# Kernel tuning notes

Hardware: AMD Instinct MI355X
Metric: run time of the kernel (lower is better)

Reference implementation:

```python
import jax, jax.numpy as jnp
import numpy as np


def _lstm(x, Wk, Wr, b):
    # x: [B, T, D] -> hidden sequence [B, T, U] (Keras LSTM gate order i,f,c,o)
    B, T, D = x.shape
    U = Wr.shape[0]
    xz = jnp.einsum('btd,dk->btk', x, Wk) + b  # precompute input projection

    def step(carry, z_t):
        h, c = carry
        z = z_t + h @ Wr
        i, f, g, o = jnp.split(z, 4, axis=-1)
        i = jax.nn.sigmoid(i)
        f = jax.nn.sigmoid(f)
        g = jnp.tanh(g)
        o = jax.nn.sigmoid(o)
        c = f * c + i * g
        h = o * jnp.tanh(c)
        return (h, c), h

    h0 = jnp.zeros((B, U), x.dtype)
    (_, _), hs = jax.lax.scan(step, (h0, h0), jnp.swapaxes(xz, 0, 1))
    return jnp.swapaxes(hs, 0, 1)


def _bilstm(x, fk, fr, fb, bk, br, bb, return_sequences):
    fwd = _lstm(x, fk, fr, fb)
    bwd = _lstm(x[:, ::-1], bk, br, bb)
    if return_sequences:
        return jnp.concatenate([fwd, bwd[:, ::-1]], axis=-1)
    return jnp.concatenate([fwd[:, -1], bwd[:, -1]], axis=-1)


def setup_inputs() -> dict:
    key = jax.random.key(0)
    ks = jax.random.split(key, 20)
    B, T, H, M, F = 64, 512, 768, 50, 8
    s = 0.05
    inp = {
        'hidden': jax.random.normal(ks[0], (B, T, H), jnp.float32),
        'mask': jax.random.randint(ks[1], (B, T), 0, M, jnp.int32),
        'lstm_input': jax.random.normal(ks[2], (B, M, F), jnp.float32),
        'max_len': M,
        'l1f_k': s * jax.random.normal(ks[3], (H + F, 4 * 256), jnp.float32),
        'l1f_r': s * jax.random.normal(ks[4], (256, 4 * 256), jnp.float32),
        'l1f_b': jnp.zeros((4 * 256,), jnp.float32),
        'l1b_k': s * jax.random.normal(ks[5], (H + F, 4 * 256), jnp.float32),
        'l1b_r': s * jax.random.normal(ks[6], (256, 4 * 256), jnp.float32),
        'l1b_b': jnp.zeros((4 * 256,), jnp.float32),
        'l2f_k': s * jax.random.normal(ks[7], (512, 4 * 128), jnp.float32),
        'l2f_r': s * jax.random.normal(ks[8], (128, 4 * 128), jnp.float32),
        'l2f_b': jnp.zeros((4 * 128,), jnp.float32),
        'l2b_k': s * jax.random.normal(ks[9], (512, 4 * 128), jnp.float32),
        'l2b_r': s * jax.random.normal(ks[10], (128, 4 * 128), jnp.float32),
        'l2b_b': jnp.zeros((4 * 128,), jnp.float32),
        'd1_w': s * jax.random.normal(ks[11], (256, 128), jnp.float32),
        'd1_b': jnp.zeros((128,), jnp.float32),
        'd3_w': s * jax.random.normal(ks[12], (128, 64), jnp.float32),
        'd3_b': jnp.zeros((64,), jnp.float32),
        'd5_w': s * jax.random.normal(ks[13], (64, 32), jnp.float32),
        'd5_b': jnp.zeros((32,), jnp.float32),
        'd7_w': s * jax.random.normal(ks[14], (32, 1), jnp.float32),
        'd7_b': jnp.zeros((1,), jnp.float32),
    }
    return inp


def reference(hidden, mask, lstm_input, max_len,
              l1f_k, l1f_r, l1f_b, l1b_k, l1b_r, l1b_b,
              l2f_k, l2f_r, l2f_b, l2b_k, l2b_r, l2b_b,
              d1_w, d1_b, d3_w, d3_b, d5_w, d5_b, d7_w, d7_b):
    # Segment reduce: for each bin d in [0, max_len), sum hidden states whose
    # mask==d, divided by max_len (the original divides by max_len, not counts).
    onehot = (mask[:, :, None] == jnp.arange(max_len)[None, None, :]).astype(hidden.dtype)
    merged = jnp.einsum('btd,btm->bmd', hidden, onehot) / jnp.asarray(max_len, hidden.dtype)
    concat = jnp.concatenate([merged, lstm_input], axis=2)  # [B, max_len, 768+F]
    out = _bilstm(concat, l1f_k, l1f_r, l1f_b, l1b_k, l1b_r, l1b_b, True)   # [B, M, 512]
    out = _bilstm(out, l2f_k, l2f_r, l2f_b, l2b_k, l2b_r, l2b_b, False)      # [B, 256]
    out = jax.nn.relu(out @ d1_w + d1_b)
    out = jax.nn.relu(out @ d3_w + d3_b)
    out = jax.nn.relu(out @ d5_w + d5_b)
    return jax.nn.sigmoid(out @ d7_w + d7_b)  # [B, 1]
```

## Files before the change

kernel.cpp:

```cpp
#include <hip/hip_runtime.h>
#include <hip/hip_bf16.h>

typedef __attribute__((ext_vector_type(8))) short bf16x8;
typedef __attribute__((ext_vector_type(4))) float f32x4;
typedef __attribute__((ext_vector_type(4))) unsigned int u32x4;
typedef _Float16 half2_ __attribute__((ext_vector_type(2)));

__device__ __forceinline__ unsigned short f2bf(float f) {
    unsigned int x = __float_as_uint(f);
    x += 0x7fffu + ((x >> 16) & 1u);
    return (unsigned short)(x >> 16);
}

__device__ __forceinline__ float sigmoidf_(float x) {
    return 1.f / (1.f + __expf(-x));
}
__device__ __forceinline__ float tanhf_(float x) {
    float e = __expf(-2.f * fabsf(x));
    float t = (1.f - e) / (1.f + e);
    return copysignf(t, x);
}

__device__ __forceinline__ float fdot2_(unsigned int w, unsigned int h, float acc) {
#if __has_builtin(__builtin_amdgcn_fdot2)
    return __builtin_amdgcn_fdot2(__builtin_bit_cast(half2_, w),
                                  __builtin_bit_cast(half2_, h), acc, false);
#else
    half2_ a = __builtin_bit_cast(half2_, w);
    half2_ b = __builtin_bit_cast(half2_, h);
    return acc + (float)a.x * (float)b.x + (float)a.y * (float)b.y;
#endif
}

__device__ void convT_body(const float* __restrict__ srcF,
                           const float* __restrict__ srcB,
                           short* __restrict__ dst, int Ksrc, int Kpad,
                           int Nhalf, int bx, int by, float* tile ) {
    int k0 = bx * 64, n0 = by * 64;
    const float* src = (n0 < Nhalf) ? srcF : srcB;
    int ncol0 = (n0 < Nhalf) ? n0 : n0 - Nhalf;
    int c = threadIdx.x & 63;
    int r4 = threadIdx.x >> 6;
    for (int rr = r4; rr < 64; rr += 4) {
        int k = k0 + rr;
        tile[rr * 65 + c] = (k < Ksrc) ? src[(size_t)k * Nhalf + ncol0 + c] : 0.f;
    }
    __syncthreads();
    int rn = threadIdx.x >> 2, q = threadIdx.x & 3;
    short* d = dst + (size_t)(n0 + rn) * Kpad + k0 + q * 16;
    #pragma unroll
    for (int i = 0; i < 16; i++) d[i] = (short)f2bf(tile[(q * 16 + i) * 65 + rn]);
}

__device__ void conv_rec_pack_body(const float* __restrict__ WrF,
                                   const float* __restrict__ WrB,
                                   unsigned int* __restrict__ dst, int K, int N,
                                   int kq, int dir) {
    const float* src = dir ? WrB : WrF;
    int kqq = kq >> 2, q = kq & 3;
    for (int c = threadIdx.x; c < N; c += 256) {
        half2_ h;
        h.x = (_Float16)src[(size_t)(2 * kq) * N + c];
        h.y = (_Float16)src[(size_t)(2 * kq + 1) * N + c];
        dst[(((size_t)dir * (K / 8) + kqq) * N + c) * 4 + q] =
            __builtin_bit_cast(unsigned int, h);
    }
}

__device__ void onehot_body(const int* __restrict__ mask,
                            const float* __restrict__ lstm_in,
                            short* __restrict__ onehot,
                            short* __restrict__ concatB, int b) {
    int tid = threadIdx.x;
    short* oh = onehot + (size_t)b * 64 * 512;
    for (int i = tid; i < 64 * 512 / 8; i += 256) {
        bf16x8 z = {};
        *(bf16x8*)(oh + i * 8) = z;
    }
    __syncthreads();
    for (int t = tid; t < 512; t += 256) {
        unsigned int m = (unsigned int)mask[b * 512 + t];
        if (m < 50u) oh[(size_t)m * 512 + t] = (short)0x3F80;
    }
    for (int idx = tid; idx < 50 * 64; idx += 256) {
        int m = idx >> 6, q = idx & 63;
        float v = (q < 8) ? lstm_in[(b * 50 + m) * 8 + q] : 0.f;
        concatB[(size_t)(b * 50 + m) * 832 + 768 + q] = (short)f2bf(v);
    }
}

__global__ __launch_bounds__(256) void prep_all(
    const float* __restrict__ l1f_k, const float* __restrict__ l1b_k,
    short* __restrict__ wk1T,
    const float* __restrict__ l2f_k, const float* __restrict__ l2b_k,
    short* __restrict__ wk2T,
    const float* __restrict__ l1f_r, const float* __restrict__ l1b_r,
    unsigned int* __restrict__ wp1,
    const float* __restrict__ l2f_r, const float* __restrict__ l2b_r,
    unsigned int* __restrict__ wp2,
    const int* __restrict__ mask, const float* __restrict__ lstm_in,
    short* __restrict__ onehot, short* __restrict__ concatB) {
    __shared__ float tile[64 * 65];
    int blk = blockIdx.x;
    if (blk < 416) {
        convT_body(l1f_k, l1b_k, wk1T, 776, 832, 1024, blk % 13, blk / 13, tile);
    } else if (blk < 544) {
        int q = blk - 416;
        convT_body(l2f_k, l2b_k, wk2T, 512, 512, 512, q % 8, q / 8, tile);
    } else if (blk < 800) {
        int q = blk - 544;
        conv_rec_pack_body(l1f_r, l1b_r, wp1, 256, 1024, q & 127, q >> 7);
    } else if (blk < 928) {
        int q = blk - 800;
        conv_rec_pack_body(l2f_r, l2b_r, wp2, 128, 512, q & 63, q >> 6);
    } else {
        onehot_body(mask, lstm_in, onehot, concatB, blk - 928);
    }
}

__global__ __launch_bounds__(256) void seg_gemm(
    const float* __restrict__ hidden, const short* __restrict__ onehot,
    short* __restrict__ concatB) {
    int b = blockIdx.x, n0 = blockIdx.y * 64;
    __shared__ short Al[64][36];
    __shared__ short Bl[64][36];
    int tid = threadIdx.x;
    int lane = tid & 63, w = tid >> 6;
    int fr = lane & 15, fq = lane >> 4;
    int wc = w * 16;
    int arow = tid >> 2, apart = tid & 3;
    int nloc = tid & 63, kq = tid >> 6;

    f32x4 acc[4] = {};

    const short* ohb = onehot + (size_t)b * 64 * 512;
    const float* hbase = hidden + (size_t)b * 512 * 768 + n0 + nloc;

    bf16x8 aReg = *(const bf16x8*)(ohb + (size_t)arow * 512 + apart * 8);
    float bReg[8];
    #pragma unroll
    for (int kk = 0; kk < 8; kk++)
        bReg[kk] = hbase[(size_t)(kq * 8 + kk) * 768];

    for (int k0 = 0; k0 < 512; k0 += 32) {
        *(bf16x8*)&Al[arow][apart * 8] = aReg;
        #pragma unroll
        for (int kk = 0; kk < 8; kk += 2) {
            unsigned int pk = (unsigned int)f2bf(bReg[kk]) |
                              ((unsigned int)f2bf(bReg[kk + 1]) << 16);
            *(unsigned int*)&Bl[nloc][kq * 8 + kk] = pk;
        }
        __syncthreads();
        if (k0 + 32 < 512) {
            int kn = k0 + 32;
            aReg = *(const bf16x8*)(ohb + (size_t)arow * 512 + kn + apart * 8);
            #pragma unroll
            for (int kk = 0; kk < 8; kk++)
                bReg[kk] = hbase[(size_t)(kn + kq * 8 + kk) * 768];
        }
        bf16x8 af[4], bfv;
        #pragma unroll
        for (int mi = 0; mi < 4; mi++)
            af[mi] = *(const bf16x8*)&Al[mi * 16 + fr][fq * 8];
        bfv = *(const bf16x8*)&Bl[wc + fr][fq * 8];
        #pragma unroll
        for (int mi = 0; mi < 4; mi++)
            acc[mi] = __builtin_amdgcn_mfma_f32_16x16x32_bf16(af[mi], bfv,
                                                              acc[mi], 0, 0, 0);
        __syncthreads();
    }
    const float inv = 1.f / 50.f;
    #pragma unroll
    for (int mi = 0; mi < 4; mi++) {
        #pragma unroll
        for (int r = 0; r < 4; r++) {
            int m = mi * 16 + fq * 4 + r;
            if (m < 50) {
                int col = n0 + wc + fr;
                concatB[(size_t)(b * 50 + m) * 832 + col] =
                    (short)f2bf(acc[mi][r] * inv);
            }
        }
    }
}

__global__ __launch_bounds__(256) void gemm_bf16(
    const short* __restrict__ A, const short* __restrict__ BT,
    const float* __restrict__ biasF, const float* __restrict__ biasB, int Nhalf,
    float* __restrict__ C, int M, int N, int Kpad) {
    __shared__ short Al[128][72];
    __shared__ short Bl[128][72];
    int m0 = blockIdx.x * 128, n0 = blockIdx.y * 128;
    int tid = threadIdx.x;
    int lane = tid & 63, w = tid >> 6;
    int srow = tid >> 1, shalf = tid & 1;
    int wr = (w >> 1) * 64, wc = (w & 1) * 64;
    int fr = lane & 15, fq = lane >> 4;

    f32x4 acc[4][4] = {};

    const short* aPtr = A + (size_t)(m0 + srow) * Kpad + shalf * 32;
    const short* bPtr = BT + (size_t)(n0 + srow) * Kpad + shalf * 32;
    bf16x8 av0 = *(const bf16x8*)(aPtr);
    bf16x8 av1 = *(const bf16x8*)(aPtr + 16);
    bf16x8 bv0 = *(const bf16x8*)(bPtr);
    bf16x8 bv1 = *(const bf16x8*)(bPtr + 16);

    for (int k0 = 0; k0 < Kpad; k0 += 64) {
        *(bf16x8*)&Al[srow][shalf * 32] = av0;
        *(bf16x8*)&Al[srow][shalf * 32 + 16] = av1;
        *(bf16x8*)&Bl[srow][shalf * 32] = bv0;
        *(bf16x8*)&Bl[srow][shalf * 32 + 16] = bv1;
        __syncthreads();
        if (k0 + 64 < Kpad) {
            av0 = *(const bf16x8*)(aPtr + k0 + 64);
            av1 = *(const bf16x8*)(aPtr + k0 + 80);
            bv0 = *(const bf16x8*)(bPtr + k0 + 64);
            bv1 = *(const bf16x8*)(bPtr + k0 + 80);
        }
        #pragma unroll
        for (int ks = 0; ks < 2; ks++) {
            bf16x8 af[4], bfv[4];
            #pragma unroll
            for (int mi = 0; mi < 4; mi++)
                af[mi] = *(const bf16x8*)&Al[wr + mi * 16 + fr][ks * 32 + fq * 8];
            #pragma unroll
            for (int ni = 0; ni < 4; ni++)
                bfv[ni] = *(const bf16x8*)&Bl[wc + ni * 16 + fr][ks * 32 + fq * 8];
            #pragma unroll
            for (int mi = 0; mi < 4; mi++)
                #pragma unroll
                for (int ni = 0; ni < 4; ni++)
                    acc[mi][ni] = __builtin_amdgcn_mfma_f32_16x16x32_bf16(
                        af[mi], bfv[ni], acc[mi][ni], 0, 0, 0);
        }
        __syncthreads();
    }
    #pragma unroll
    for (int mi = 0; mi < 4; mi++)
        #pragma unroll
        for (int ni = 0; ni < 4; ni++) {
            #pragma unroll
            for (int r = 0; r < 4; r++) {
                int row = m0 + wr + mi * 16 + fq * 4 + r;
                int col = n0 + wc + ni * 16 + fr;
                float bias = (col < Nhalf) ? biasF[col] : biasB[col - Nhalf];
                C[(size_t)row * N + col] = acc[mi][ni][r] + bias;
            }
        }
}

#define R1_REG 25
#define R1_LDS 7

__global__ __attribute__((amdgpu_flat_work_group_size(512, 512)))
__attribute__((amdgpu_waves_per_eu(2, 2))) void lstm_rec1(
    const float* __restrict__ xz, const unsigned int* __restrict__ wp,
    short* __restrict__ out1) {
    int b = blockIdx.x >> 1, dir = blockIdx.x & 1;
    const unsigned int* wd = wp + (size_t)dir * 32 * 1024 * 4;
    extern __shared__ char smem[];
    unsigned int* Wl = (unsigned int*)smem;
    unsigned int* h2u = (unsigned int*)(smem + R1_LDS * 1024 * 16);
    float* zbuf = (float*)(smem + R1_LDS * 1024 * 16 + 512);
    int tid = threadIdx.x;
    int lane = tid & 63;
    int cA = tid, cB = tid + 512;

    unsigned int wA[R1_REG * 4], wB[R1_REG * 4];
    #pragma unroll
    for (int g = 0; g < R1_REG; g++) {
        u32x4 ta = *(const u32x4*)&wd[((size_t)g * 1024 + cA) * 4];
        u32x4 tb = *(const u32x4*)&wd[((size_t)g * 1024 + cB) * 4];
        wA[g * 4 + 0] = ta.x; wA[g * 4 + 1] = ta.y;
        wA[g * 4 + 2] = ta.z; wA[g * 4 + 3] = ta.w;
        wB[g * 4 + 0] = tb.x; wB[g * 4 + 1] = tb.y;
        wB[g * 4 + 2] = tb.z; wB[g * 4 + 3] = tb.w;
    }
    #pragma unroll
    for (int g = 0; g < R1_REG; g++) {
        asm volatile("" : "+v"(wA[g * 4 + 0]), "+v"(wA[g * 4 + 1]),
                          "+v"(wA[g * 4 + 2]), "+v"(wA[g * 4 + 3]),
                          "+v"(wB[g * 4 + 0]), "+v"(wB[g * 4 + 1]),
                          "+v"(wB[g * 4 + 2]), "+v"(wB[g * 4 + 3]));
    }
    #pragma unroll
    for (int g = 0; g < R1_LDS; g++) {
        *(u32x4*)&Wl[(g * 1024 + cA) * 4] =
            *(const u32x4*)&wd[((size_t)(R1_REG + g) * 1024 + cA) * 4];
        *(u32x4*)&Wl[(g * 1024 + cB) * 4] =
            *(const u32x4*)&wd[((size_t)(R1_REG + g) * 1024 + cB) * 4];
    }
    if (tid < 128) h2u[tid] = 0u;
    float cstate = 0.f;
    __syncthreads();

    for (int s = 0; s < 50; s++) {
        int tt = dir ? 49 - s : s;
        const float* xrow = xz + (size_t)(b * 50 + tt) * 2048 + dir * 1024;
        float xA = xrow[cA];
        float xB = xrow[cB];
        float zA0 = 0.f, zA1 = 0.f, zA2 = 0.f, zA3 = 0.f;
        float zB0 = 0.f, zB1 = 0.f, zB2 = 0.f, zB3 = 0.f;
        unsigned int hv0 = h2u[lane];
        unsigned int hv1 = h2u[lane + 64];
        #pragma unroll
        for (int g = 0; g < R1_REG; g++) {
            unsigned int src = (g < 16) ? hv0 : hv1;
            int base = (g < 16) ? 4 * g : 4 * (g - 16);
            unsigned int h0 = __builtin_amdgcn_readlane(src, base + 0);
            unsigned int h1 = __builtin_amdgcn_readlane(src, base + 1);
            unsigned int h2 = __builtin_amdgcn_readlane(src, base + 2);
            unsigned int h3 = __builtin_amdgcn_readlane(src, base + 3);
            zA0 = fdot2_(wA[g * 4 + 0], h0, zA0);
            zA1 = fdot2_(wA[g * 4 + 1], h1, zA1);
            zA2 = fdot2_(wA[g * 4 + 2], h2, zA2);
            zA3 = fdot2_(wA[g * 4 + 3], h3, zA3);
            zB0 = fdot2_(wB[g * 4 + 0], h0, zB0);
            zB1 = fdot2_(wB[g * 4 + 1], h1, zB1);
            zB2 = fdot2_(wB[g * 4 + 2], h2, zB2);
            zB3 = fdot2_(wB[g * 4 + 3], h3, zB3);
        }
        #pragma unroll
        for (int g = 0; g < R1_LDS; g++) {
            int gg = R1_REG + g;
            int base = 4 * (gg - 16);
            unsigned int h0 = __builtin_amdgcn_readlane(hv1, base + 0);
            unsigned int h1 = __builtin_amdgcn_readlane(hv1, base + 1);
            unsigned int h2 = __builtin_amdgcn_readlane(hv1, base + 2);
            unsigned int h3 = __builtin_amdgcn_readlane(hv1, base + 3);
            u32x4 wa = *(const u32x4*)&Wl[(g * 1024 + cA) * 4];
            u32x4 wb = *(const u32x4*)&Wl[(g * 1024 + cB) * 4];
            zA0 = fdot2_(wa.x, h0, zA0);
            zA1 = fdot2_(wa.y, h1, zA1);
            zA2 = fdot2_(wa.z, h2, zA2);
            zA3 = fdot2_(wa.w, h3, zA3);
            zB0 = fdot2_(wb.x, h0, zB0);
            zB1 = fdot2_(wb.y, h1, zB1);
            zB2 = fdot2_(wb.z, h2, zB2);
            zB3 = fdot2_(wb.w, h3, zB3);
        }
        zbuf[cA] = (zA0 + zA1) + (zA2 + zA3) + xA;
        zbuf[cB] = (zB0 + zB1) + (zB2 + zB3) + xB;
        __syncthreads();
        if (tid < 256) {
            float iv = sigmoidf_(zbuf[tid]);
            float fv = sigmoidf_(zbuf[tid + 256]);
            float gv = tanhf_(zbuf[tid + 512]);
            float ov = sigmoidf_(zbuf[tid + 768]);
            cstate = fv * cstate + iv * gv;
            float h = ov * tanhf_(cstate);
            ((_Float16*)h2u)[tid] = (_Float16)h;
            out1[(size_t)(b * 50 + tt) * 512 + dir * 256 + tid] = (short)f2bf(h);
        }
        __syncthreads();
    }
}

__global__ __launch_bounds__(512, 2) void lstm_rec2(
    const float* __restrict__ xz, const unsigned int* __restrict__ wp,
    float* __restrict__ out2) {
    int b = blockIdx.x >> 1, dir = blockIdx.x & 1;
    const unsigned int* wd = wp + (size_t)dir * 16 * 512 * 4;
    __shared__ unsigned int h2u[64];
    __shared__ float zbuf[512];
    int tid = threadIdx.x;
    int lane = tid & 63;
    unsigned int w[64];
    #pragma unroll
    for (int g = 0; g < 16; g++) {
        u32x4 t = *(const u32x4*)&wd[((size_t)g * 512 + tid) * 4];
        w[g * 4 + 0] = t.x; w[g * 4 + 1] = t.y;
        w[g * 4 + 2] = t.z; w[g * 4 + 3] = t.w;
    }
    #pragma unroll
    for (int g = 0; g < 16; g++) {
        asm volatile("" : "+v"(w[g * 4 + 0]), "+v"(w[g * 4 + 1]),
                          "+v"(w[g * 4 + 2]), "+v"(w[g * 4 + 3]));
    }
    if (tid < 64) h2u[tid] = 0u;
    float cstate = 0.f;
    __syncthreads();

    for (int s = 0; s < 50; s++) {
        int tt = dir ? 49 - s : s;
        float xv = xz[(size_t)(b * 50 + tt) * 1024 + dir * 512 + tid];
        float z0 = 0.f, z1 = 0.f, z2 = 0.f, z3 = 0.f;
        unsigned int hv = h2u[lane];
        #pragma unroll
        for (int g = 0; g < 16; g++) {
            unsigned int h0 = __builtin_amdgcn_readlane(hv, 4 * g + 0);
            unsigned int h1 = __builtin_amdgcn_readlane(hv, 4 * g + 1);
            unsigned int h2 = __builtin_amdgcn_readlane(hv, 4 * g + 2);
            unsigned int h3 = __builtin_amdgcn_readlane(hv, 4 * g + 3);
            z0 = fdot2_(w[g * 4 + 0], h0, z0);
            z1 = fdot2_(w[g * 4 + 1], h1, z1);
            z2 = fdot2_(w[g * 4 + 2], h2, z2);
            z3 = fdot2_(w[g * 4 + 3], h3, z3);
        }
        zbuf[tid] = (z0 + z1) + (z2 + z3) + xv;
        __syncthreads();
        if (tid < 128) {
            float iv = sigmoidf_(zbuf[tid]);
            float fv = sigmoidf_(zbuf[tid + 128]);
            float gv = tanhf_(zbuf[tid + 256]);
            float ov = sigmoidf_(zbuf[tid + 384]);
            cstate = fv * cstate + iv * gv;
            float h = ov * tanhf_(cstate);
            ((_Float16*)h2u)[tid] = (_Float16)h;
            if (s == 49) out2[b * 256 + dir * 128 + tid] = h;
        }
        __syncthreads();
    }
}

__global__ __launch_bounds__(128) void dense_head(
    const float* __restrict__ out2,
    const float* __restrict__ d1w, const float* __restrict__ d1b,
    const float* __restrict__ d3w, const float* __restrict__ d3b,
    const float* __restrict__ d5w, const float* __restrict__ d5b,
    const float* __restrict__ d7w, const float* __restrict__ d7b,
    float* __restrict__ out) {
    int b = blockIdx.x;
    int tid = threadIdx.x;
    __shared__ float x[256], y1[128], y2[64], y3[32];
    x[tid] = out2[b * 256 + tid];
    x[tid + 128] = out2[b * 256 + tid + 128];
    __syncthreads();
    {
        float a = d1b[tid];
        for (int k = 0; k < 256; k++) a = fmaf(x[k], d1w[k * 128 + tid], a);
        y1[tid] = fmaxf(a, 0.f);
    }
    __syncthreads();
    if (tid < 64) {
        float a = d3b[tid];
        for (int k = 0; k < 128; k++) a = fmaf(y1[k], d3w[k * 64 + tid], a);
        y2[tid] = fmaxf(a, 0.f);
    }
    __syncthreads();
    if (tid < 32) {
        float a = d5b[tid];
        for (int k = 0; k < 64; k++) a = fmaf(y2[k], d5w[k * 32 + tid], a);
        y3[tid] = fmaxf(a, 0.f);
    }
    __syncthreads();
    if (tid == 0) {
        float a = d7b[0];
        for (int k = 0; k < 32; k++) a = fmaf(y3[k], d7w[k], a);
        out[b] = 1.f / (1.f + __expf(-a));
    }
}

extern "C" void kernel_launch(void* const* d_in, const int* in_sizes, int n_in,
                              void* d_out, int out_size, void* d_ws, size_t ws_size,
                              hipStream_t stream) {
    const float* hidden  = (const float*)d_in[0];
    const int*   mask    = (const int*)d_in[1];
    const float* lstm_in = (const float*)d_in[2];
    const float* l1f_k = (const float*)d_in[4];
    const float* l1f_r = (const float*)d_in[5];
    const float* l1f_b = (const float*)d_in[6];
    const float* l1b_k = (const float*)d_in[7];
    const float* l1b_r = (const float*)d_in[8];
    const float* l1b_b = (const float*)d_in[9];
    const float* l2f_k = (const float*)d_in[10];
    const float* l2f_r = (const float*)d_in[11];
    const float* l2f_b = (const float*)d_in[12];
    const float* l2b_k = (const float*)d_in[13];
    const float* l2b_r = (const float*)d_in[14];
    const float* l2b_b = (const float*)d_in[15];
    const float* d1w = (const float*)d_in[16];
    const float* d1b = (const float*)d_in[17];
    const float* d3w = (const float*)d_in[18];
    const float* d3b = (const float*)d_in[19];
    const float* d5w = (const float*)d_in[20];
    const float* d5b = (const float*)d_in[21];
    const float* d7w = (const float*)d_in[22];
    const float* d7b = (const float*)d_in[23];

    char* p = (char*)d_ws;
    short* concatB = (short*)p; p += (size_t)3200 * 832 * 2;
    short* wk1T    = (short*)p; p += (size_t)2048 * 832 * 2;
    short* wk2T    = (short*)p; p += (size_t)1024 * 512 * 2;
    float* xz1     = (float*)p; p += (size_t)3200 * 2048 * 4;
    short* out1    = (short*)p; p += (size_t)3200 * 512 * 2;
    float* xz2     = (float*)p; p += (size_t)3200 * 1024 * 4;
    float* out2    = (float*)p; p += (size_t)64 * 256 * 4;
    unsigned int* wp1 = (unsigned int*)p; p += (size_t)2 * 32 * 1024 * 4 * 4;
    unsigned int* wp2 = (unsigned int*)p; p += (size_t)2 * 16 * 512 * 4 * 4;
    short* onehot  = (short*)p; p += (size_t)64 * 64 * 512 * 2;

    const int lds1 = R1_LDS * 1024 * 16 + 512 + 4096;
    hipFuncSetAttribute((const void*)lstm_rec1,
                        hipFuncAttributeMaxDynamicSharedMemorySize, lds1);

    prep_all<<<992, 256, 0, stream>>>(l1f_k, l1b_k, wk1T, l2f_k, l2b_k, wk2T,
                                      l1f_r, l1b_r, wp1, l2f_r, l2b_r, wp2,
                                      mask, lstm_in, onehot, concatB);
    seg_gemm<<<dim3(64, 12), 256, 0, stream>>>(hidden, onehot, concatB);
    gemm_bf16<<<dim3(25, 16), 256, 0, stream>>>(concatB, wk1T, l1f_b, l1b_b, 1024,
                                                xz1, 3200, 2048, 832);
    lstm_rec1<<<128, 512, lds1, stream>>>(xz1, wp1, out1);
    gemm_bf16<<<dim3(25, 8), 256, 0, stream>>>(out1, wk2T, l2f_b, l2b_b, 512,
                                               xz2, 3200, 1024, 512);
    lstm_rec2<<<128, 512, 0, stream>>>(xz2, wp2, out2);
    dense_head<<<64, 128, 0, stream>>>(out2, d1w, d1b, d3w, d3b, d5w, d5b,
                                       d7w, d7b, (float*)d_out);
}
```

Before: 222.7 us.

## Build one-hot operands in registers and split layer-2 recurrence K across 1024 threads

The segment-sum GEMM no longer materialises a one-hot bf16 matrix in global memory. Instead it loads the mask into LDS and builds the one-hot A fragments in registers, which removes the zero-fill, the scatter and the A-tile reads. Separately, the second LSTM recurrence now runs 1024 threads per block, with each half handling half of the K dimension and partial sums combined through LDS. This halves the per-thread serial dot-product chain per step, at the cost of an extra LDS reduction and fewer waves of occupancy headroom.

Result: slower. 235.1 us (+5.6%).

```diff
diff --git a/kernel.cpp b/kernel.cpp
--- a/kernel.cpp
+++ b/kernel.cpp
@@ -67,21 +67,9 @@
     }
 }
 
-__device__ void onehot_body(const int* __restrict__ mask,
-                            const float* __restrict__ lstm_in,
-                            short* __restrict__ onehot,
+__device__ void concat_body(const float* __restrict__ lstm_in,
                             short* __restrict__ concatB, int b) {
     int tid = threadIdx.x;
-    short* oh = onehot + (size_t)b * 64 * 512;
-    for (int i = tid; i < 64 * 512 / 8; i += 256) {
-        bf16x8 z = {};
-        *(bf16x8*)(oh + i * 8) = z;
-    }
-    __syncthreads();
-    for (int t = tid; t < 512; t += 256) {
-        unsigned int m = (unsigned int)mask[b * 512 + t];
-        if (m < 50u) oh[(size_t)m * 512 + t] = (short)0x3F80;
-    }
     for (int idx = tid; idx < 50 * 64; idx += 256) {
         int m = idx >> 6, q = idx & 63;
         float v = (q < 8) ? lstm_in[(b * 50 + m) * 8 + q] : 0.f;
@@ -98,8 +86,7 @@
     unsigned int* __restrict__ wp1,
     const float* __restrict__ l2f_r, const float* __restrict__ l2b_r,
     unsigned int* __restrict__ wp2,
-    const int* __restrict__ mask, const float* __restrict__ lstm_in,
-    short* __restrict__ onehot, short* __restrict__ concatB) {
+    const float* __restrict__ lstm_in, short* __restrict__ concatB) {
     __shared__ float tile[64 * 65];
     int blk = blockIdx.x;
     if (blk < 416) {
@@ -114,36 +101,33 @@
         int q = blk - 800;
         conv_rec_pack_body(l2f_r, l2b_r, wp2, 128, 512, q & 63, q >> 6);
     } else {
-        onehot_body(mask, lstm_in, onehot, concatB, blk - 928);
+        concat_body(lstm_in, concatB, blk - 928);
     }
 }
 
 __global__ __launch_bounds__(256) void seg_gemm(
-    const float* __restrict__ hidden, const short* __restrict__ onehot,
+    const float* __restrict__ hidden, const int* __restrict__ mask,
     short* __restrict__ concatB) {
     int b = blockIdx.x, n0 = blockIdx.y * 64;
-    __shared__ short Al[64][36];
     __shared__ short Bl[64][36];
+    __shared__ int mloc[512];
     int tid = threadIdx.x;
     int lane = tid & 63, w = tid >> 6;
     int fr = lane & 15, fq = lane >> 4;
     int wc = w * 16;
-    int arow = tid >> 2, apart = tid & 3;
     int nloc = tid & 63, kq = tid >> 6;
 
+    for (int i = tid; i < 512; i += 256) mloc[i] = mask[b * 512 + i];
+
     f32x4 acc[4] = {};
-
-    const short* ohb = onehot + (size_t)b * 64 * 512;
     const float* hbase = hidden + (size_t)b * 512 * 768 + n0 + nloc;
 
-    bf16x8 aReg = *(const bf16x8*)(ohb + (size_t)arow * 512 + apart * 8);
     float bReg[8];
     #pragma unroll
     for (int kk = 0; kk < 8; kk++)
         bReg[kk] = hbase[(size_t)(kq * 8 + kk) * 768];
 
     for (int k0 = 0; k0 < 512; k0 += 32) {
-        *(bf16x8*)&Al[arow][apart * 8] = aReg;
         #pragma unroll
         for (int kk = 0; kk < 8; kk += 2) {
             unsigned int pk = (unsigned int)f2bf(bReg[kk]) |
@@ -153,15 +137,18 @@
         __syncthreads();
         if (k0 + 32 < 512) {
             int kn = k0 + 32;
-            aReg = *(const bf16x8*)(ohb + (size_t)arow * 512 + kn + apart * 8);
             #pragma unroll
             for (int kk = 0; kk < 8; kk++)
                 bReg[kk] = hbase[(size_t)(kn + kq * 8 + kk) * 768];
         }
         bf16x8 af[4], bfv;
         #pragma unroll
-        for (int mi = 0; mi < 4; mi++)
-            af[mi] = *(const bf16x8*)&Al[mi * 16 + fr][fq * 8];
+        for (int j = 0; j < 8; j++) {
+            int mk = mloc[k0 + fq * 8 + j];
+            #pragma unroll
+            for (int mi = 0; mi < 4; mi++)
+                af[mi][j] = (mk == mi * 16 + fr) ? (short)0x3F80 : (short)0;
+        }
         bfv = *(const bf16x8*)&Bl[wc + fr][fq * 8];
         #pragma unroll
         for (int mi = 0; mi < 4; mi++)
@@ -357,24 +344,25 @@
     }
 }
 
-__global__ __launch_bounds__(512, 2) void lstm_rec2(
+__global__ __launch_bounds__(1024) void lstm_rec2(
     const float* __restrict__ xz, const unsigned int* __restrict__ wp,
     float* __restrict__ out2) {
     int b = blockIdx.x >> 1, dir = blockIdx.x & 1;
     const unsigned int* wd = wp + (size_t)dir * 16 * 512 * 4;
     __shared__ unsigned int h2u[64];
-    __shared__ float zbuf[512];
+    __shared__ float part[2][512];
     int tid = threadIdx.x;
     int lane = tid & 63;
-    unsigned int w[64];
-    #pragma unroll
-    for (int g = 0; g < 16; g++) {
-        u32x4 t = *(const u32x4*)&wd[((size_t)g * 512 + tid) * 4];
+    int c = tid & 511, kh = tid >> 9;
+    unsigned int w[32];
+    #pragma unroll
+    for (int g = 0; g < 8; g++) {
+        u32x4 t = *(const u32x4*)&wd[((size_t)(kh * 8 + g) * 512 + c) * 4];
         w[g * 4 + 0] = t.x; w[g * 4 + 1] = t.y;
         w[g * 4 + 2] = t.z; w[g * 4 + 3] = t.w;
     }
     #pragma unroll
-    for (int g = 0; g < 16; g++) {
+    for (int g = 0; g < 8; g++) {
         asm volatile("" : "+v"(w[g * 4 + 0]), "+v"(w[g * 4 + 1]),
                           "+v"(w[g * 4 + 2]), "+v"(w[g * 4 + 3]));
     }
@@ -384,27 +372,29 @@
 
     for (int s = 0; s < 50; s++) {
         int tt = dir ? 49 - s : s;
-        float xv = xz[(size_t)(b * 50 + tt) * 1024 + dir * 512 + tid];
-        float z0 = 0.f, z1 = 0.f, z2 = 0.f, z3 = 0.f;
+        float z0 = (kh == 0) ? xz[(size_t)(b * 50 + tt) * 1024 + dir * 512 + c]
+                             : 0.f;
+        float z1 = 0.f, z2 = 0.f, z3 = 0.f;
         unsigned int hv = h2u[lane];
         #pragma unroll
-        for (int g = 0; g < 16; g++) {
-            unsigned int h0 = __builtin_amdgcn_readlane(hv, 4 * g + 0);
-            unsigned int h1 = __builtin_amdgcn_readlane(hv, 4 * g + 1);
-            unsigned int h2 = __builtin_amdgcn_readlane(hv, 4 * g + 2);
-            unsigned int h3 = __builtin_amdgcn_readlane(hv, 4 * g + 3);
+        for (int g = 0; g < 8; g++) {
+            int gg = kh * 8 + g;
+            unsigned int h0 = __builtin_amdgcn_readlane(hv, 4 * gg + 0);
+            unsigned int h1 = __builtin_amdgcn_readlane(hv, 4 * gg + 1);
+            unsigned int h2 = __builtin_amdgcn_readlane(hv, 4 * gg + 2);
+            unsigned int h3 = __builtin_amdgcn_readlane(hv, 4 * gg + 3);
             z0 = fdot2_(w[g * 4 + 0], h0, z0);
             z1 = fdot2_(w[g * 4 + 1], h1, z1);
             z2 = fdot2_(w[g * 4 + 2], h2, z2);
             z3 = fdot2_(w[g * 4 + 3], h3, z3);
         }
-        zbuf[tid] = (z0 + z1) + (z2 + z3) + xv;
+        part[kh][c] = (z0 + z1) + (z2 + z3);
         __syncthreads();
         if (tid < 128) {
-            float iv = sigmoidf_(zbuf[tid]);
-            float fv = sigmoidf_(zbuf[tid + 128]);
-            float gv = tanhf_(zbuf[tid + 256]);
-            float ov = sigmoidf_(zbuf[tid + 384]);
+            float iv = sigmoidf_(part[0][tid] + part[1][tid]);
+            float fv = sigmoidf_(part[0][tid + 128] + part[1][tid + 128]);
+            float gv = tanhf_(part[0][tid + 256] + part[1][tid + 256]);
+            float ov = sigmoidf_(part[0][tid + 384] + part[1][tid + 384]);
             cstate = fv * cstate + iv * gv;
             float h = ov * tanhf_(cstate);
             ((_Float16*)h2u)[tid] = (_Float16)h;
@@ -489,7 +479,6 @@
     float* out2    = (float*)p; p += (size_t)64 * 256 * 4;
     unsigned int* wp1 = (unsigned int*)p; p += (size_t)2 * 32 * 1024 * 4 * 4;
     unsigned int* wp2 = (unsigned int*)p; p += (size_t)2 * 16 * 512 * 4 * 4;
-    short* onehot  = (short*)p; p += (size_t)64 * 64 * 512 * 2;
 
     const int lds1 = R1_LDS * 1024 * 16 + 512 + 4096;
     hipFuncSetAttribute((const void*)lstm_rec1,
@@ -497,14 +486,14 @@
 
     prep_all<<<992, 256, 0, stream>>>(l1f_k, l1b_k, wk1T, l2f_k, l2b_k, wk2T,
                                       l1f_r, l1b_r, wp1, l2f_r, l2b_r, wp2,
-                                      mask, lstm_in, onehot, concatB);
-    seg_gemm<<<dim3(64, 12), 256, 0, stream>>>(hidden, onehot, concatB);
+                                      lstm_in, concatB);
+    seg_gemm<<<dim3(64, 12), 256, 0, stream>>>(hidden, mask, concatB);
     gemm_bf16<<<dim3(25, 16), 256, 0, stream>>>(concatB, wk1T, l1f_b, l1b_b, 1024,
                                                 xz1, 3200, 2048, 832);
     lstm_rec1<<<128, 512, lds1, stream>>>(xz1, wp1, out1);
     gemm_bf16<<<dim3(25, 8), 256, 0, stream>>>(out1, wk2T, l2f_b, l2b_b, 512,
                                                xz2, 3200, 1024, 512);
-    lstm_rec2<<<128, 512, 0, stream>>>(xz2, wp2, out2);
+    lstm_rec2<<<128, 1024, 0, stream>>>(xz2, wp2, out2);
     dense_head<<<64, 128, 0, stream>>>(out2, d1w, d1b, d3w, d3b, d5w, d5b,
                                        d7w, d7b, (float*)d_out);
 }
```
